# Performance work log

Hardware: AMD Instinct MI355X
Metric: run time of the kernel (lower is better)

Reference implementation:

```python
import jax, jax.numpy as jnp
import numpy as np
from jax import lax

EPS = 1e-12
N_ITER = 25
PAD = 1
GROUPS = 4


def conv2d(x, w, padding, groups):
    # x: NCHW, w: OIHW (I = C // groups)
    return lax.conv_general_dilated(
        x, w, (1, 1), ((padding, padding), (padding, padding)),
        dimension_numbers=('NCHW', 'OIHW', 'NCHW'), feature_group_count=groups)


def conv_transpose2d(h, w, padding, groups):
    # stride-1 transposed conv == conv with spatially flipped, in/out-swapped kernel
    O, Ig, kh, kw = w.shape
    I = Ig * groups
    wt = w.reshape(groups, O // groups, Ig, kh, kw).transpose(0, 2, 1, 3, 4)
    wt = wt.reshape(I, O // groups, kh, kw)[:, :, ::-1, ::-1]
    return conv2d(h, wt, kh - 1 - padding, groups)


def nnmf_conv2d(x, weight, n_iterations=N_ITER, padding=PAD, groups=GROUPS,
                normalize_channels=True):
    # non-negative, L1-normalized (per output channel) weights
    w = jnp.abs(weight)
    w = w / (w.sum(axis=(1, 2, 3), keepdims=True) + EPS)
    # non-negative input, normalized over channels
    x = x / (x.sum(axis=1, keepdims=True) + EPS)
    N, C, H, W = x.shape
    O = weight.shape[0]
    h0 = jnp.full((N, O, H, W), 1.0 / O, dtype=x.dtype)

    def body(i, h):
        recon = conv_transpose2d(h, w, padding, groups)   # back-projection
        ratio = x / (recon + EPS)
        h = h * conv2d(ratio, w, padding, groups)         # multiplicative update
        if normalize_channels:
            h = h / (h.sum(axis=1, keepdims=True) + EPS)
        return h

    return lax.fori_loop(0, n_iterations, body, h0)


def layernorm_cf(x, w, b, eps=1e-6):
    # channels_first LayerNorm over C of NCHW
    u = x.mean(axis=1, keepdims=True)
    s = jnp.mean((x - u) ** 2, axis=1, keepdims=True)
    xn = (x - u) * lax.rsqrt(s + eps)
    return w[None, :, None, None] * xn + b[None, :, None, None]


def layernorm_last(x, w, b, eps=1e-5):
    u = x.mean(axis=-1, keepdims=True)
    s = jnp.mean((x - u) ** 2, axis=-1, keepdims=True)
    return (x - u) * lax.rsqrt(s + eps) * w + b


def setup_inputs() -> dict:
    key = jax.random.key(0)
    ks = jax.random.split(key, 8)
    C, Hd = 96, 384  # dim, mlp hidden = 4*embed_dim
    x = jax.random.normal(ks[0], (8, C, 56, 56), dtype=jnp.float32)
    return {
        'x': x,
        'ln1_w': jnp.ones((C,), jnp.float32),
        'ln1_b': jnp.zeros((C,), jnp.float32),
        'w_nnmf': jax.random.uniform(ks[1], (C, C // GROUPS, 3, 3), jnp.float32, 0.01, 1.0),
        'ln2_w': jnp.ones((C,), jnp.float32),
        'ln2_b': jnp.zeros((C,), jnp.float32),
        'w1': jax.random.normal(ks[2], (C, Hd), jnp.float32) * 0.02,
        'b1': jnp.zeros((Hd,), jnp.float32),
        'w2': jax.random.normal(ks[3], (Hd, C), jnp.float32) * 0.02,
        'b2': jnp.zeros((C,), jnp.float32),
    }


def reference(x, ln1_w, ln1_b, w_nnmf, ln2_w, ln2_b, w1, b1, w2, b2):
    # attn branch (NNMF conv on relu'd channels-first layernorm)
    x_norm = layernorm_cf(x, ln1_w, ln1_b)
    x = x + nnmf_conv2d(jax.nn.relu(x_norm), w_nnmf)
    # MLP branch, channels-last
    xl = jnp.transpose(x, (0, 2, 3, 1))  # NHWC
    h = layernorm_last(xl, ln2_w, ln2_b)
    h = jax.nn.gelu(h @ w1 + b1, approximate=False) @ w2 + b2
    xl = xl + h
    return jnp.transpose(xl, (0, 3, 1, 2))
```

## Files before the change

kernel.cpp:

```cpp
#include <hip/hip_runtime.h>
#include <math.h>
#include <string.h>

typedef unsigned short ushort_t;
typedef __attribute__((ext_vector_type(8))) short bhalf8;
typedef __attribute__((ext_vector_type(4))) float floatx4;

#define NN    8
#define CC_   96
#define HH    56
#define WW    56
#define HWHW  (HH*WW)
#define NPIX  (NN*HWHW)
#define NELEM (NN*CC_*HWHW)
#define GROUPS 4
#define IG    24
#define NITER 25
#define EPSV  1e-12f
#define TS    40

__device__ __forceinline__ unsigned bf2pack(float a, float b) {
    unsigned ua = __float_as_uint(a), ub = __float_as_uint(b);
    ua += 0x7fffu + ((ua >> 16) & 1u);
    ub += 0x7fffu + ((ub >> 16) & 1u);
    return (ua >> 16) | (ub & 0xffff0000u);
}
__device__ __forceinline__ ushort_t bf1pack(float a) {
    unsigned ua = __float_as_uint(a);
    ua += 0x7fffu + ((ua >> 16) & 1u);
    return (ushort_t)(ua >> 16);
}
__device__ __forceinline__ float bflo(unsigned u) { return __uint_as_float(u << 16); }
__device__ __forceinline__ float bfhi(unsigned u) { return __uint_as_float(u & 0xffff0000u); }

__device__ __forceinline__ float rcpf(float x) {
    float r;
    asm("v_rcp_f32 %0, %1" : "=v"(r) : "v"(x));
    return r;
}

__device__ __forceinline__ int swz(int slot, int u) {
    return slot*TS + ((((u >> 3) ^ (slot >> 3)) & 3) << 3) + (u & 7);
}

__global__ __launch_bounds__(256) void prep_kernel(
        const float* __restrict__ w_in,
        ushort_t* __restrict__ WfP, ushort_t* __restrict__ WtP,
        const float* __restrict__ w1, const float* __restrict__ w2,
        ushort_t* __restrict__ w1P, ushort_t* __restrict__ w2P,
        const float* __restrict__ x, const float* __restrict__ lw1,
        const float* __restrict__ lb1, unsigned* __restrict__ Xp) {
    __shared__ float wn[24*216];
    __shared__ float rsum[24];
    int b = blockIdx.x;
    int tid = threadIdx.x;

    if (b < 4) {
        int g = b;
        if (tid < 24) {
            const float* wr = w_in + (size_t)(g*24 + tid)*216;
            float s = 0.f;
            for (int j = 0; j < 216; ++j) s += fabsf(wr[j]);
            rsum[tid] = s;
        }
        __syncthreads();
        for (int i = tid; i < 24*216; i += 256) {
            int row = i / 216;
            wn[i] = fabsf(w_in[(size_t)g*24*216 + i]) * rcpf(rsum[row] + EPSV);
        }
        __syncthreads();
        int lg = tid >> 6;
        int lane = tid & 63;
        int quad = lane >> 4, nn15 = lane & 15;
        #pragma unroll 1
        for (int i = 0; i < 9; ++i) {
            int fr  = lg + 4*i;
            int sel = fr / 18;
            int rem = fr % 18;
            int ot  = rem & 1;
            int tap = rem >> 1;
            int m = ot*16 + nn15;
            ushort_t v[8];
            #pragma unroll
            for (int j = 0; j < 8; ++j) {
                int kc = quad*8 + j;
                float val = 0.f;
                if (m < IG && kc < IG) {
                    if (sel == 0) val = wn[m*216 + kc*9 + tap];
                    else          val = wn[kc*216 + m*9 + (8 - tap)];
                }
                v[j] = bf1pack(val);
            }
            ushort_t* dst = (sel ? WtP : WfP) + ((size_t)((g*9 + tap)*2 + ot)*64 + lane)*8;
            *(uint4*)dst = *(uint4*)v;
        }
    } else if (b < 40) {
        int f = (b - 4)*4 + (tid >> 6);
        int lane = tid & 63;
        int quad = lane >> 4, nn15 = lane & 15;
        ushort_t v[8];
        if (f < 72) {
            int nt = f / 3, ks = f % 3;
            #pragma unroll
            for (int j = 0; j < 8; ++j)
                v[j] = bf1pack(w1[(size_t)(ks*32 + quad*8 + j)*384 + nt*16 + nn15]);
            *(uint4*)(w1P + ((size_t)f*64 + lane)*8) = *(uint4*)v;
        } else {
            int f2 = f - 72;
            int mt = f2 / 12, ks = f2 % 12;
            #pragma unroll
            for (int j = 0; j < 8; ++j)
                v[j] = bf1pack(w2[(size_t)(ks*32 + quad*8 + j)*96 + mt*16 + nn15]);
            *(uint4*)(w2P + ((size_t)f2*64 + lane)*8) = *(uint4*)v;
        }
    } else {
        int p = (b - 40)*256 + tid;
        int n = p / HWHW, hw = p % HWHW;
        const float* xp = x + (size_t)n*CC_*HWHW + hw;
        float s = 0.f, ss = 0.f;
        for (int c = 0; c < CC_; ++c) { float v = xp[(size_t)c*HWHW]; s += v; ss += v*v; }
        float u  = s * (1.f/CC_);
        float var = ss * (1.f/CC_) - u*u;
        float rs = rsqrtf(var + 1e-6f);
        float sr = 0.f;
        for (int c = 0; c < CC_; ++c) {
            float v = xp[(size_t)c*HWHW];
            float a = fmaxf((v-u)*rs*lw1[c] + lb1[c], 0.f);
            sr += a;
        }
        float inv = 1.f / (sr + EPSV);
        for (int c = 0; c < CC_; c += 2) {
            float v0 = xp[(size_t)c*HWHW];
            float v1 = xp[(size_t)(c+1)*HWHW];
            float a0 = fmaxf((v0-u)*rs*lw1[c] + lb1[c], 0.f) * inv;
            float a1 = fmaxf((v1-u)*rs*lw1[c+1] + lb1[c+1], 0.f) * inv;
            int g = c / IG, pr = (c % IG) >> 1;
            Xp[(size_t)((n*4+g)*12 + pr)*HWHW + hw] = bf2pack(a0, a1);
        }
    }
}

__global__ __launch_bounds__(512, 4) void nnmf_mfma_kernel(
        const unsigned* __restrict__ HupI, unsigned* __restrict__ HupO,
        const float* __restrict__ Scur, float* __restrict__ Snxt,
        const ushort_t* __restrict__ WtP, const ushort_t* __restrict__ WfP,
        const unsigned* __restrict__ Xp,
        int it0, unsigned huInit, float sInit) {
    __shared__ ushort_t hn[352*TS];
    __shared__ ushort_t rt_[288*TS];
    __shared__ float sacc[392];
    int b    = blockIdx.x;
    int k_   = b >> 3;
    int ng   = (b & 7)*4 + (k_ >> 4);
    int tile = k_ & 15;
    int rtb  = tile >> 1;
    int half = tile & 1;
    int n    = ng >> 2;
    int g    = ng & 3;
    int tid  = threadIdx.x;
    int r0   = rtb*7;
    int xb   = half*28;
    unsigned planeBase = (unsigned)(n*4 + g)*12;

    int waveId = tid >> 6, lane = tid & 63;
    int quad = lane >> 4, nn = lane & 15;
    int otB = waveId & 1;
    int mbB = otB*16 + quad*4;

    bhalf8 afrB[9];
    {
        const ushort_t* ap = WtP + ((size_t)(g*9*2 + otB)*64 + lane)*8;
        #pragma unroll
        for (int t = 0; t < 9; ++t) afrB[t] = *(const bhalf8*)(ap + (size_t)t*2*64*8);
    }

    uint2 raw[6];
    float sA[6], sB[6], sC[6], sD[6];
    #pragma unroll
    for (int kk = 0; kk < 6; ++kk) {
        int idx = tid + kk*512;
        uint2 rv = {0u, 0u};
        float a0 = 0.f, a1 = 0.f, a2 = 0.f, a3 = 0.f;
        if (idx < 2816) {
            int pr2  = idx / 352;
            int slot = idx - pr2*352;
            int r = slot >> 5, q = slot & 31;
            int gr = r0 - 2 + r, gc = xb - 2 + q;
            if (!it0 && pr2 < 6 && gr >= 0 && gr < HH && gc >= 0 && gc < WW) {
                unsigned off = (unsigned)(gr*WW + gc);
                unsigned pix = (unsigned)(n*HWHW) + off;
                rv.x = HupI[(size_t)(planeBase + 2*pr2)*HWHW + off];
                rv.y = HupI[(size_t)(planeBase + 2*pr2 + 1)*HWHW + off];
                a0 = Scur[pix];
                a1 = Scur[NPIX + pix];
                a2 = Scur[2*NPIX + pix];
                a3 = Scur[3*NPIX + pix];
            }
        }
        raw[kk] = rv;
        sA[kk] = a0; sB[kk] = a1; sC[kk] = a2; sD[kk] = a3;
    }

    #pragma unroll
    for (int kk = 0; kk < 6; ++kk) {
        int idx = tid + kk*512;
        if (idx < 2816) {
            int pr2  = idx / 352;
            int slot = idx - pr2*352;
            int r = slot >> 5, q = slot & 31;
            int gr = r0 - 2 + r, gc = xb - 2 + q;
            uint2 pk = {0u, 0u};
            if (pr2 < 6 && gr >= 0 && gr < HH && gc >= 0 && gc < WW) {
                if (it0) {
                    float si = rcpf(4.f*sInit + EPSV);
                    float hval = bflo(huInit) * si;
                    pk.x = bf2pack(hval, hval);
                    pk.y = pk.x;
                } else {
                    float st = sA[kk] + sB[kk] + sC[kk] + sD[kk];
                    float si = rcpf(st + EPSV);
                    pk.x = bf2pack(bflo(raw[kk].x)*si, bfhi(raw[kk].x)*si);
                    pk.y = bf2pack(bflo(raw[kk].y)*si, bfhi(raw[kk].y)*si);
                }
            }
            *(uint2*)&hn[swz(slot, 4*pr2)] = pk;
        }
    }
    if (tid < 288) *(uint4*)&rt_[swz(tid, 24)] = (uint4){0u,0u,0u,0u};
    __syncthreads();

    {
        #pragma unroll
        for (int i = 0; i < 5; ++i) {
            int tk = waveId + 8*i;
            if (tk < 36) {
                int pt  = (tk >> 1) & 1;
                int row = tk >> 2;
                int x0R = pt*14;
                unsigned xa = 0u, xc = 0u;
                int gr = r0 - 1 + row, gc = xb - 1 + x0R + nn;
                if (mbB < IG && gr >= 0 && gr < HH && gc >= 0 && gc < WW) {
                    unsigned off = (unsigned)(gr*WW + gc);
                    unsigned pb = planeBase + (unsigned)(mbB >> 1);
                    xa = Xp[(size_t)pb*HWHW + off];
                    xc = Xp[(size_t)(pb+1)*HWHW + off];
                }
                floatx4 acc = (floatx4){0.f,0.f,0.f,0.f};
                #pragma unroll
                for (int t = 0; t < 9; ++t) {
                    int ky = t / 3, kx = t % 3;
                    bhalf8 bfr = *(const bhalf8*)
                        &hn[swz((row + ky)*32 + kx + nn + x0R, quad*8)];
                    acc = __builtin_amdgcn_mfma_f32_16x16x32_bf16(afrB[t], bfr, acc, 0, 0, 0);
                }
                if (mbB < IG) {
                    int slot = row*32 + x0R + nn;
                    *(unsigned*)&rt_[swz(slot, mbB)] =
                        bf2pack(bflo(xa)*rcpf(acc[0]+EPSV), bfhi(xa)*rcpf(acc[1]+EPSV));
                    *(unsigned*)&rt_[swz(slot, mbB + 2)] =
                        bf2pack(bflo(xc)*rcpf(acc[2]+EPSV), bfhi(xc)*rcpf(acc[3]+EPSV));
                }
            }
        }
    }
    __syncthreads();

    {
        const ushort_t* ap = WfP + ((size_t)(g*9*2 + otB)*64 + lane)*8;
        bhalf8 afr[9];
        #pragma unroll
        for (int t = 0; t < 9; ++t) afr[t] = *(const bhalf8*)(ap + (size_t)t*2*64*8);
        int mb = mbB;

        #pragma unroll
        for (int i = 0; i < 4; ++i) {
            int tc = waveId + 8*i;
            if (tc < 28) {
                int xt = (tc >> 1) & 1;
                int w  = tc >> 2;
                int px0 = xt*12;
                floatx4 acc = (floatx4){0.f,0.f,0.f,0.f};
                #pragma unroll
                for (int t = 0; t < 9; ++t) {
                    int ky = t / 3, kx = t % 3;
                    bhalf8 bfr = *(const bhalf8*)
                        &rt_[swz((w + ky)*32 + kx + nn + px0, quad*8)];
                    acc = __builtin_amdgcn_mfma_f32_16x16x32_bf16(afr[t], bfr, acc, 0, 0, 0);
                }

                int grow = r0 + w;
                int pxh = px0 + nn;
                float psum = 0.f;
                if (mb < IG) {
                    unsigned off = (unsigned)(grow*WW + xb + pxh);
                    unsigned pb = planeBase + (unsigned)(mb >> 1);
                    uint2 hv = *(const uint2*)&hn[swz((w + 2)*32 + pxh + 2, mb)];
                    float h0 = bflo(hv.x) * acc[0];
                    float h1 = bfhi(hv.x) * acc[1];
                    float h2 = bflo(hv.y) * acc[2];
                    float h3 = bfhi(hv.y) * acc[3];
                    HupO[(size_t)pb*HWHW + off]     = bf2pack(h0, h1);
                    HupO[(size_t)(pb+1)*HWHW + off] = bf2pack(h2, h3);
                    psum = h0 + h1 + h2 + h3;
                }
                psum += __shfl_down(psum, 32, 64);
                psum += __shfl_down(psum, 16, 64);
                if (lane < 16) sacc[otB*196 + w*28 + pxh] = psum;
            }
        }
    }
    __syncthreads();
    if (tid < 196) {
        Snxt[(size_t)g*NPIX + n*HWHW + (r0 + tid/28)*WW + xb + (tid % 28)]
            = sacc[tid] + sacc[196 + tid];
    }
}

__global__ __launch_bounds__(128) void mlpres_kernel(
        const float* __restrict__ x, const unsigned* __restrict__ Hup,
        const float* __restrict__ S4,
        const float* __restrict__ lw, const float* __restrict__ lb,
        const ushort_t* __restrict__ w1P, const float* __restrict__ b1,
        const ushort_t* __restrict__ w2P, const float* __restrict__ b2,
        float* __restrict__ out) {
    __shared__ ushort_t lh[16*392];
    __shared__ unsigned xln[16*52];
    __shared__ float vt[96*18];
    __shared__ float redS[8*16], redSS[8*16];
    __shared__ float uArr[16], rsArr[16];
    int blk = blockIdx.x;
    int tid = threadIdx.x;
    int p0  = blk * 16;
    int n   = p0 / HWHW;
    int hw0 = p0 % HWHW;

    {
        int px = tid & 15, cg = tid >> 4;
        int p  = p0 + px, hw = hw0 + px;
        float stot = S4[p] + S4[NPIX+p] + S4[2*NPIX+p] + S4[3*NPIX+p];
        float sinv = 1.f / (stot + EPSV);
        int g = cg >> 1;
        unsigned plane = (unsigned)(n*4 + g)*12 + (unsigned)((cg & 1)*6);
        size_t xbase = (size_t)n*CC_*HWHW + hw;
        float v[12];
        float s = 0.f, ss = 0.f;
        #pragma unroll
        for (int j = 0; j < 6; ++j) {
            int c = cg*12 + 2*j;
            unsigned hu = Hup[(size_t)(plane + j)*HWHW + hw];
            float v0 = x[xbase + (size_t)c*HWHW]     + bflo(hu) * sinv;
            float v1 = x[xbase + (size_t)(c+1)*HWHW] + bfhi(hu) * sinv;
            v[2*j] = v0; v[2*j+1] = v1;
            s += v0 + v1; ss += v0*v0 + v1*v1;
        }
        redS[cg*16 + px] = s; redSS[cg*16 + px] = ss;
        __syncthreads();
        if (tid < 16) {
            float S_ = 0.f, SS_ = 0.f;
            #pragma unroll
            for (int k = 0; k < 8; ++k) { S_ += redS[k*16 + tid]; SS_ += redSS[k*16 + tid]; }
            float u  = S_ * (1.f/CC_);
            float var = SS_ * (1.f/CC_) - u*u;
            uArr[tid] = u; rsArr[tid] = rsqrtf(var + 1e-5f);
        }
        __syncthreads();
        float u = uArr[px], rs = rsArr[px];
        #pragma unroll
        for (int j = 0; j < 6; ++j) {
            int c = cg*12 + 2*j;
            float a0 = (v[2*j]   - u)*rs*lw[c]   + lb[c];
            float a1 = (v[2*j+1] - u)*rs*lw[c+1] + lb[c+1];
            xln[px*52 + cg*6 + j] = bf2pack(a0, a1);
            vt[c*18 + px]     = v[2*j];
            vt[(c+1)*18 + px] = v[2*j+1];
        }
    }
    __syncthreads();

    int wv  = tid >> 6, lane = tid & 63;
    int quad = lane >> 4, nn = lane & 15;

    bhalf8 a1[3];
    #pragma unroll
    for (int ks = 0; ks < 3; ++ks)
        a1[ks] = *(const bhalf8*)&xln[nn*52 + ks*16 + quad*4];

    #pragma unroll 1
    for (int i = 0; i < 12; ++i) {
        int nt = wv*12 + i;
        floatx4 acc = (floatx4){0.f,0.f,0.f,0.f};
        #pragma unroll
        for (int ks = 0; ks < 3; ++ks) {
            bhalf8 bfr = *(const bhalf8*)(w1P + ((size_t)(nt*3 + ks)*64 + lane)*8);
            acc = __builtin_amdgcn_mfma_f32_16x16x32_bf16(a1[ks], bfr, acc, 0, 0, 0);
        }
        float b1v = b1[nt*16 + nn];
        #pragma unroll
        for (int r = 0; r < 4; ++r) {
            float h = acc[r] + b1v;
            h = 0.5f * h * (1.f + erff(h * 0.70710678118654752440f));
            lh[(quad*4 + r)*392 + nt*16 + nn] = bf1pack(h);
        }
    }
    __syncthreads();

    bhalf8 bf2[12];
    #pragma unroll
    for (int ks = 0; ks < 12; ++ks)
        bf2[ks] = *(const bhalf8*)&lh[nn*392 + ks*32 + quad*8];

    #pragma unroll 1
    for (int i = 0; i < 3; ++i) {
        int mt = wv*3 + i;
        floatx4 acc = (floatx4){0.f,0.f,0.f,0.f};
        #pragma unroll
        for (int ks = 0; ks < 12; ++ks) {
            bhalf8 af = *(const bhalf8*)(w2P + ((size_t)(mt*12 + ks)*64 + lane)*8);
            acc = __builtin_amdgcn_mfma_f32_16x16x32_bf16(af, bf2[ks], acc, 0, 0, 0);
        }
        #pragma unroll
        for (int r = 0; r < 4; ++r) {
            int c = mt*16 + quad*4 + r;
            size_t addr = ((size_t)n*CC_ + c)*HWHW + hw0 + nn;
            out[addr] = vt[c*18 + nn] + (acc[r] + b2[c]);
        }
    }
}

extern "C" void kernel_launch(void* const* d_in, const int* in_sizes, int n_in,
                              void* d_out, int out_size, void* d_ws, size_t ws_size,
                              hipStream_t stream) {
    const float* x    = (const float*)d_in[0];
    const float* ln1w = (const float*)d_in[1];
    const float* ln1b = (const float*)d_in[2];
    const float* wnn  = (const float*)d_in[3];
    const float* ln2w = (const float*)d_in[4];
    const float* ln2b = (const float*)d_in[5];
    const float* w1   = (const float*)d_in[6];
    const float* b1   = (const float*)d_in[7];
    const float* w2   = (const float*)d_in[8];
    const float* b2   = (const float*)d_in[9];
    float* out = (float*)d_out;
    char* ws = (char*)d_ws;

    ushort_t* WfP  = (ushort_t*)ws;                   ws += 73728*2;
    ushort_t* WtP  = (ushort_t*)ws;                   ws += 73728*2;
    ushort_t* w1P  = (ushort_t*)ws;                   ws += 36864*2;
    ushort_t* w2P  = (ushort_t*)ws;                   ws += 36864*2;
    unsigned* Xp   = (unsigned*)ws;                   ws += (size_t)(NELEM/2)*4;
    unsigned* Hu0  = (unsigned*)ws;                   ws += (size_t)(NELEM/2)*4;
    unsigned* Hu1  = (unsigned*)ws;                   ws += (size_t)(NELEM/2)*4;
    float*    SA   = (float*)ws;                      ws += (size_t)4*NPIX*4;
    float*    SB   = (float*)ws;                      ws += (size_t)4*NPIX*4;

    union { float f; unsigned u; } cv; cv.f = 1.f/96.f;
    unsigned ur = cv.u + 0x7fffu + ((cv.u >> 16) & 1u);
    unsigned short hbits = (unsigned short)(ur >> 16);
    unsigned huInit = ((unsigned)hbits << 16) | hbits;
    union { float f; unsigned u; } hv; hv.u = ((unsigned)hbits) << 16;
    float sInit = 24.f * hv.f;

    prep_kernel<<<138, 256, 0, stream>>>(wnn, WfP, WtP, w1, w2, w1P, w2P,
                                         x, ln1w, ln1b, Xp);

    for (int it = 0; it < NITER; ++it) {
        const unsigned* HuI  = (it & 1) ? Hu1 : Hu0;
        unsigned*       HuO  = (it & 1) ? Hu0 : Hu1;
        const float*    Scur = (it & 1) ? SB : SA;
        float*          Snxt = (it & 1) ? SA : SB;
        nnmf_mfma_kernel<<<512, 512, 0, stream>>>(HuI, HuO, Scur, Snxt, WtP, WfP, Xp,
                                                  (it == 0) ? 1 : 0, huInit, sInit);
    }

    mlpres_kernel<<<NPIX/16, 128, 0, stream>>>(x, Hu1, SB, ln2w, ln2b,
                                               w1P, b1, w2P, b2, out);
}
```

Baseline: 402.7 us.

## Interleave bf16 channel quads and group sums for vectorized global access

Changes the layout of the packed input, the iterate H and the per-group sum buffer. Groups of four channels are now stored together per pixel (uint2) and the four group sums are interleaved per pixel (float4), replacing the earlier split-plane layout. Each of these accesses becomes one wider load or store instead of two or four scalar ones, which cuts memory instructions in the 25-iteration loop and the MLP kernel. Every producer and consumer has to agree on the new indexing, and any part of the code not updated would read wrong data.

```diff
diff --git a/kernel.cpp b/kernel.cpp
--- a/kernel.cpp
+++ b/kernel.cpp
@@ -129,13 +129,16 @@
             sr += a;
         }
         float inv = 1.f / (sr + EPSV);
-        for (int c = 0; c < CC_; c += 2) {
-            float v0 = xp[(size_t)c*HWHW];
-            float v1 = xp[(size_t)(c+1)*HWHW];
-            float a0 = fmaxf((v0-u)*rs*lw1[c] + lb1[c], 0.f) * inv;
-            float a1 = fmaxf((v1-u)*rs*lw1[c+1] + lb1[c+1], 0.f) * inv;
-            int g = c / IG, pr = (c % IG) >> 1;
-            Xp[(size_t)((n*4+g)*12 + pr)*HWHW + hw] = bf2pack(a0, a1);
+        for (int c = 0; c < CC_; c += 4) {
+            float a[4];
+            #pragma unroll
+            for (int j = 0; j < 4; ++j) {
+                float v = xp[(size_t)(c+j)*HWHW];
+                a[j] = fmaxf((v-u)*rs*lw1[c+j] + lb1[c+j], 0.f) * inv;
+            }
+            int g = c / IG, pr2 = (c % IG) >> 2;
+            uint2 pk; pk.x = bf2pack(a[0], a[1]); pk.y = bf2pack(a[2], a[3]);
+            *(uint2*)&Xp[2*(((size_t)(n*4+g)*6 + pr2)*HWHW + hw)] = pk;
         }
     }
 }
@@ -160,7 +163,7 @@
     int tid  = threadIdx.x;
     int r0   = rtb*7;
     int xb   = half*28;
-    unsigned planeBase = (unsigned)(n*4 + g)*12;
+    unsigned plane6 = (unsigned)(n*4 + g)*6;
 
     int waveId = tid >> 6, lane = tid & 63;
     int quad = lane >> 4, nn = lane & 15;
@@ -175,12 +178,12 @@
     }
 
     uint2 raw[6];
-    float sA[6], sB[6], sC[6], sD[6];
+    float sSum[6];
     #pragma unroll
     for (int kk = 0; kk < 6; ++kk) {
         int idx = tid + kk*512;
         uint2 rv = {0u, 0u};
-        float a0 = 0.f, a1 = 0.f, a2 = 0.f, a3 = 0.f;
+        float st = 0.f;
         if (idx < 2816) {
             int pr2  = idx / 352;
             int slot = idx - pr2*352;
@@ -189,16 +192,13 @@
             if (!it0 && pr2 < 6 && gr >= 0 && gr < HH && gc >= 0 && gc < WW) {
                 unsigned off = (unsigned)(gr*WW + gc);
                 unsigned pix = (unsigned)(n*HWHW) + off;
-                rv.x = HupI[(size_t)(planeBase + 2*pr2)*HWHW + off];
-                rv.y = HupI[(size_t)(planeBase + 2*pr2 + 1)*HWHW + off];
-                a0 = Scur[pix];
-                a1 = Scur[NPIX + pix];
-                a2 = Scur[2*NPIX + pix];
-                a3 = Scur[3*NPIX + pix];
+                rv = *(const uint2*)&HupI[2*((size_t)(plane6 + pr2)*HWHW + off)];
+                float4 sv = *(const float4*)&Scur[4*(size_t)pix];
+                st = sv.x + sv.y + sv.z + sv.w;
             }
         }
         raw[kk] = rv;
-        sA[kk] = a0; sB[kk] = a1; sC[kk] = a2; sD[kk] = a3;
+        sSum[kk] = st;
     }
 
     #pragma unroll
@@ -217,8 +217,7 @@
                     pk.x = bf2pack(hval, hval);
                     pk.y = pk.x;
                 } else {
-                    float st = sA[kk] + sB[kk] + sC[kk] + sD[kk];
-                    float si = rcpf(st + EPSV);
+                    float si = rcpf(sSum[kk] + EPSV);
                     pk.x = bf2pack(bflo(raw[kk].x)*si, bfhi(raw[kk].x)*si);
                     pk.y = bf2pack(bflo(raw[kk].y)*si, bfhi(raw[kk].y)*si);
                 }
@@ -241,9 +240,8 @@
                 int gr = r0 - 1 + row, gc = xb - 1 + x0R + nn;
                 if (mbB < IG && gr >= 0 && gr < HH && gc >= 0 && gc < WW) {
                     unsigned off = (unsigned)(gr*WW + gc);
-                    unsigned pb = planeBase + (unsigned)(mbB >> 1);
-                    xa = Xp[(size_t)pb*HWHW + off];
-                    xc = Xp[(size_t)(pb+1)*HWHW + off];
+                    uint2 xv = *(const uint2*)&Xp[2*((size_t)(plane6 + (mbB >> 2))*HWHW + off)];
+                    xa = xv.x; xc = xv.y;
                 }
                 floatx4 acc = (floatx4){0.f,0.f,0.f,0.f};
                 #pragma unroll
@@ -293,14 +291,13 @@
                 float psum = 0.f;
                 if (mb < IG) {
                     unsigned off = (unsigned)(grow*WW + xb + pxh);
-                    unsigned pb = planeBase + (unsigned)(mb >> 1);
                     uint2 hv = *(const uint2*)&hn[swz((w + 2)*32 + pxh + 2, mb)];
                     float h0 = bflo(hv.x) * acc[0];
                     float h1 = bfhi(hv.x) * acc[1];
                     float h2 = bflo(hv.y) * acc[2];
                     float h3 = bfhi(hv.y) * acc[3];
-                    HupO[(size_t)pb*HWHW + off]     = bf2pack(h0, h1);
-                    HupO[(size_t)(pb+1)*HWHW + off] = bf2pack(h2, h3);
+                    uint2 po; po.x = bf2pack(h0, h1); po.y = bf2pack(h2, h3);
+                    *(uint2*)&HupO[2*((size_t)(plane6 + (mb >> 2))*HWHW + off)] = po;
                     psum = h0 + h1 + h2 + h3;
                 }
                 psum += __shfl_down(psum, 32, 64);
@@ -311,8 +308,8 @@
     }
     __syncthreads();
     if (tid < 196) {
-        Snxt[(size_t)g*NPIX + n*HWHW + (r0 + tid/28)*WW + xb + (tid % 28)]
-            = sacc[tid] + sacc[196 + tid];
+        unsigned pix = (unsigned)(n*HWHW + (r0 + tid/28)*WW + xb + (tid % 28));
+        Snxt[4*(size_t)pix + g] = sacc[tid] + sacc[196 + tid];
     }
 }
 
@@ -337,21 +334,25 @@
     {
         int px = tid & 15, cg = tid >> 4;
         int p  = p0 + px, hw = hw0 + px;
-        float stot = S4[p] + S4[NPIX+p] + S4[2*NPIX+p] + S4[3*NPIX+p];
+        float4 sv = *(const float4*)&S4[4*(size_t)p];
+        float stot = sv.x + sv.y + sv.z + sv.w;
         float sinv = 1.f / (stot + EPSV);
         int g = cg >> 1;
-        unsigned plane = (unsigned)(n*4 + g)*12 + (unsigned)((cg & 1)*6);
+        unsigned plane6 = (unsigned)(n*4 + g)*6 + (unsigned)((cg & 1)*3);
         size_t xbase = (size_t)n*CC_*HWHW + hw;
         float v[12];
         float s = 0.f, ss = 0.f;
         #pragma unroll
-        for (int j = 0; j < 6; ++j) {
-            int c = cg*12 + 2*j;
-            unsigned hu = Hup[(size_t)(plane + j)*HWHW + hw];
-            float v0 = x[xbase + (size_t)c*HWHW]     + bflo(hu) * sinv;
-            float v1 = x[xbase + (size_t)(c+1)*HWHW] + bfhi(hu) * sinv;
-            v[2*j] = v0; v[2*j+1] = v1;
-            s += v0 + v1; ss += v0*v0 + v1*v1;
+        for (int j2 = 0; j2 < 3; ++j2) {
+            int c = cg*12 + 4*j2;
+            uint2 hu = *(const uint2*)&Hup[2*((size_t)(plane6 + j2)*HWHW + hw)];
+            float h[4] = { bflo(hu.x), bfhi(hu.x), bflo(hu.y), bfhi(hu.y) };
+            #pragma unroll
+            for (int j = 0; j < 4; ++j) {
+                float vv = x[xbase + (size_t)(c+j)*HWHW] + h[j] * sinv;
+                v[4*j2 + j] = vv;
+                s += vv; ss += vv*vv;
+            }
         }
         redS[cg*16 + px] = s; redSS[cg*16 + px] = ss;
         __syncthreads();
```

Result: no change. 405.2 us (+0.6%).
